# Kernel tuning notes

Hardware: AMD Instinct MI355X
Metric: run time of the kernel (lower is better)

Reference implementation:

```python
import jax, jax.numpy as jnp
import numpy as np

BLOCK_SIZE = 64
N_EMBD = 128
N_HEAD = 4
HEAD_DIM = N_EMBD // N_HEAD  # 32


def setup_inputs() -> dict:
    key = jax.random.key(0)
    kx, kq, kk, kv = jax.random.split(key, 4)
    B, T = 4096, 64
    x = jax.random.normal(kx, (B, T, N_EMBD), dtype=jnp.float32)
    # nn.Linear(n_embd, head_dim, bias=False): stored as [out,in] in torch,
    # here kept as [in, out] = [128, 32] so projection is x @ W.
    s = 1.0 / np.sqrt(N_EMBD)
    Wq = jax.random.uniform(kq, (N_EMBD, HEAD_DIM), jnp.float32, -s, s)
    Wk = jax.random.uniform(kk, (N_EMBD, HEAD_DIM), jnp.float32, -s, s)
    Wv = jax.random.uniform(kv, (N_EMBD, HEAD_DIM), jnp.float32, -s, s)
    return {"x": x, "Wq": Wq, "Wk": Wk, "Wv": Wv}


def reference(x, Wq, Wk, Wv):
    B, T, C = x.shape
    q = x @ Wq  # [B, T, Hd]
    k = x @ Wk
    v = x @ Wv
    scale = 1.0 / jnp.sqrt(jnp.asarray(k.shape[-1], x.dtype))
    wei = jnp.einsum("btd,bsd->bts", q, k) * scale  # [B, T, T]
    causal = jnp.tril(jnp.ones((T, T), dtype=bool))
    wei = jnp.where(causal, wei, -jnp.inf)
    wei = jax.nn.softmax(wei, axis=-1)
    out = jnp.einsum("bts,bsd->btd", wei, v)  # [B, T, Hd]
    return out
```

## Files before the change

### kernel.cpp

```cpp
#include <hip/hip_runtime.h>


#define TT 64
#define CC 128
#define HD 32

typedef __bf16 bf16_t;
typedef __bf16 bf8_t __attribute__((ext_vector_type(8)));
typedef __bf16 bf4_t __attribute__((ext_vector_type(4)));
typedef float  f4_t  __attribute__((ext_vector_type(4)));

__global__ __launch_bounds__(256) void prep_weights(
    const float* __restrict__ Wq, const float* __restrict__ Wk,
    const float* __restrict__ Wv, bf16_t* __restrict__ wf)
{
  int t = blockIdx.x * 256 + threadIdx.x;
  int j    = t & 7;
  int lane = (t >> 3) & 63;
  int kt   = (t >> 9) & 3;
  int n6   = t >> 11;
  int k    = kt * 32 + (lane >> 4) * 8 + j;
  int col  = (n6 & 1) * 16 + (lane & 15);
  const float* W = (n6 >> 1) == 0 ? Wq : ((n6 >> 1) == 1 ? Wk : Wv);
  float v = W[k * HD + col];
  if (n6 < 2) v *= 0.17677669529663687f;
  wf[t] = (bf16_t)v;
}

__global__ __launch_bounds__(64, 2) void head_fused(
    const float* __restrict__ x, const bf8_t* __restrict__ wf,
    float* __restrict__ out)
{
  __shared__ __align__(16) bf16_t qs[TT][40];
  __shared__ __align__(16) bf16_t ks[TT][40];
  __shared__ __align__(16) bf16_t vt[HD][72];
  __shared__ __align__(16) bf16_t ps[16][72];

  const int lane = threadIdx.x;
  const int quad = lane >> 4;
  const int l16  = lane & 15;
  const int b    = blockIdx.x;
  const float* __restrict__ xblk = x + (size_t)b * (TT * CC);
  float* __restrict__ ob = out + (size_t)b * (TT * HD);

  const f4_t zero4 = {0.f, 0.f, 0.f, 0.f};

  bf8_t wfr[24];

  auto load_tile = [&](float4* d, int i) {
    #pragma unroll
    for (int kk = 0; kk < 4; ++kk) {
      const float* s = xblk + (16 * i + l16) * CC + kk * 32 + quad * 8;
      d[2 * kk]     = *(const float4*)s;
      d[2 * kk + 1] = *(const float4*)(s + 4);
    }
  };

  auto proj_tile = [&](const float4* d, int i) {
    f4_t acc[6];
    #pragma unroll
    for (int n = 0; n < 6; ++n) acc[n] = zero4;
    #pragma unroll
    for (int kk = 0; kk < 4; ++kk) {
      float4 f0 = d[2 * kk], f1 = d[2 * kk + 1];
      bf8_t a;
      a[0] = (bf16_t)f0.x; a[1] = (bf16_t)f0.y; a[2] = (bf16_t)f0.z; a[3] = (bf16_t)f0.w;
      a[4] = (bf16_t)f1.x; a[5] = (bf16_t)f1.y; a[6] = (bf16_t)f1.z; a[7] = (bf16_t)f1.w;
      #pragma unroll
      for (int n = 0; n < 6; ++n)
        acc[n] = __builtin_amdgcn_mfma_f32_16x16x32_bf16(a, wfr[n * 4 + kk], acc[n], 0, 0, 0);
    }
    #pragma unroll
    for (int r = 0; r < 4; ++r) {
      int row = 16 * i + quad * 4 + r;
      qs[row][l16]      = (bf16_t)acc[0][r];
      qs[row][16 + l16] = (bf16_t)acc[1][r];
      ks[row][l16]      = (bf16_t)acc[2][r];
      ks[row][16 + l16] = (bf16_t)acc[3][r];
    }
    bf4_t v0 = { (bf16_t)acc[4][0], (bf16_t)acc[4][1], (bf16_t)acc[4][2], (bf16_t)acc[4][3] };
    bf4_t v1 = { (bf16_t)acc[5][0], (bf16_t)acc[5][1], (bf16_t)acc[5][2], (bf16_t)acc[5][3] };
    *(bf4_t*)&vt[l16][16 * i + quad * 4]      = v0;
    *(bf4_t*)&vt[16 + l16][16 * i + quad * 4] = v1;
  };

  float4 ta[8], tb[8];
  load_tile(ta, 0);
  #pragma unroll
  for (int t = 0; t < 24; ++t) wfr[t] = wf[t * 64 + lane];
  load_tile(tb, 1);
  proj_tile(ta, 0);
  load_tile(ta, 2);
  proj_tile(tb, 1);
  load_tile(tb, 3);
  proj_tile(ta, 2);
  proj_tile(tb, 3);

  #pragma unroll
  for (int i = 0; i < 4; ++i) {
    f4_t sc[4];
    bf8_t aq = *(const bf8_t*)&qs[16 * i + l16][quad * 8];
    #pragma unroll
    for (int j = 0; j < 4; ++j) {
      sc[j] = zero4;
      if (j <= i) {
        bf8_t bk = *(const bf8_t*)&ks[16 * j + l16][quad * 8];
        sc[j] = __builtin_amdgcn_mfma_f32_16x16x32_bf16(aq, bk, zero4, 0, 0, 0);
      }
    }
    #pragma unroll
    for (int r = 0; r < 4; ++r) {
      int rl = quad * 4 + r;
      float p[4];
      float psum = 0.f;
      #pragma unroll
      for (int j = 0; j < 4; ++j) {
        if (j <= i) {
          bool valid = (j < i) | (l16 <= rl);
          float e = __expf(sc[j][r]);
          p[j] = valid ? e : 0.f;
          psum += p[j];
        } else p[j] = 0.f;
      }
      #pragma unroll
      for (int off = 1; off < 16; off <<= 1)
        psum += __shfl_xor(psum, off);
      float inv = __builtin_amdgcn_rcpf(psum);
      #pragma unroll
      for (int j = 0; j < 4; ++j) {
        if (j <= i)             ps[rl][j * 16 + l16] = (bf16_t)(p[j] * inv);
        else if (j == (i | 1))  ps[rl][j * 16 + l16] = (bf16_t)0.f;
      }
    }
    f4_t o0 = zero4, o1 = zero4;
    #pragma unroll
    for (int kk = 0; kk <= (i >> 1); ++kk) {
      int k0 = kk * 32 + quad * 8;
      bf8_t ap  = *(const bf8_t*)&ps[l16][k0];
      bf8_t bv0 = *(const bf8_t*)&vt[l16][k0];
      bf8_t bv1 = *(const bf8_t*)&vt[16 + l16][k0];
      o0 = __builtin_amdgcn_mfma_f32_16x16x32_bf16(ap, bv0, o0, 0, 0, 0);
      o1 = __builtin_amdgcn_mfma_f32_16x16x32_bf16(ap, bv1, o1, 0, 0, 0);
    }
    #pragma unroll
    for (int r = 0; r < 4; ++r) {
      int row = 16 * i + quad * 4 + r;
      ob[row * HD + l16]      = o0[r];
      ob[row * HD + 16 + l16] = o1[r];
    }
  }
}

extern "C" void kernel_launch(void* const* d_in, const int* in_sizes, int n_in,
                              void* d_out, int out_size, void* d_ws, size_t ws_size,
                              hipStream_t stream) {
  const float* x  = (const float*)d_in[0];
  const float* Wq = (const float*)d_in[1];
  const float* Wk = (const float*)d_in[2];
  const float* Wv = (const float*)d_in[3];
  float* out = (float*)d_out;
  bf16_t* wf = (bf16_t*)d_ws;
  int B = in_sizes[0] / (TT * CC);

  prep_weights<<<dim3(48), dim3(256), 0, stream>>>(Wq, Wk, Wv, wf);
  head_fused<<<dim3(B), dim3(64), 0, stream>>>(x, (const bf8_t*)wf, out);
}
```

Baseline: 208.9 us.

## Defer softmax normalization via ones-MFMA row sums and interleave projection with attention

Replaces the per-row shuffle reduction and reciprocal scaling of probabilities with an extra MFMA against a vector of ones, so each row sum comes out of the PV matmul and normalization is applied to the output. It also reorders the schedule so the softmax/PV for the first query tiles runs before the last projection tile, overlapping the final x loads with attention work. The cost is an extra MFMA per PV step. Row sums are now taken from the bf16-rounded unnormalized probabilities, which slightly changes numerics.

```diff
diff --git a/kernel.cpp b/kernel.cpp
--- a/kernel.cpp
+++ b/kernel.cpp
@@ -44,8 +44,12 @@
   float* __restrict__ ob = out + (size_t)b * (TT * HD);
 
   const f4_t zero4 = {0.f, 0.f, 0.f, 0.f};
+  bf8_t ones8;
+  #pragma unroll
+  for (int t = 0; t < 8; ++t) ones8[t] = (bf16_t)1.0f;
 
   bf8_t wfr[24];
+  float4 ta[8], tb[8];
 
   auto load_tile = [&](float4* d, int i) {
     #pragma unroll
@@ -84,20 +88,7 @@
     *(bf4_t*)&vt[16 + l16][16 * i + quad * 4] = v1;
   };
 
-  float4 ta[8], tb[8];
-  load_tile(ta, 0);
-  #pragma unroll
-  for (int t = 0; t < 24; ++t) wfr[t] = wf[t * 64 + lane];
-  load_tile(tb, 1);
-  proj_tile(ta, 0);
-  load_tile(ta, 2);
-  proj_tile(tb, 1);
-  load_tile(tb, 3);
-  proj_tile(ta, 2);
-  proj_tile(tb, 3);
-
-  #pragma unroll
-  for (int i = 0; i < 4; ++i) {
+  auto sm_tile = [&](int i) {
     f4_t sc[4];
     bf8_t aq = *(const bf8_t*)&qs[16 * i + l16][quad * 8];
     #pragma unroll
@@ -111,44 +102,49 @@
     #pragma unroll
     for (int r = 0; r < 4; ++r) {
       int rl = quad * 4 + r;
-      float p[4];
-      float psum = 0.f;
       #pragma unroll
       for (int j = 0; j < 4; ++j) {
         if (j <= i) {
           bool valid = (j < i) | (l16 <= rl);
           float e = __expf(sc[j][r]);
-          p[j] = valid ? e : 0.f;
-          psum += p[j];
-        } else p[j] = 0.f;
-      }
-      #pragma unroll
-      for (int off = 1; off < 16; off <<= 1)
-        psum += __shfl_xor(psum, off);
-      float inv = __builtin_amdgcn_rcpf(psum);
-      #pragma unroll
-      for (int j = 0; j < 4; ++j) {
-        if (j <= i)             ps[rl][j * 16 + l16] = (bf16_t)(p[j] * inv);
-        else if (j == (i | 1))  ps[rl][j * 16 + l16] = (bf16_t)0.f;
+          ps[rl][j * 16 + l16] = (bf16_t)(valid ? e : 0.f);
+        } else if (j == (i | 1)) {
+          ps[rl][j * 16 + l16] = (bf16_t)0.f;
+        }
       }
     }
-    f4_t o0 = zero4, o1 = zero4;
+    f4_t o0 = zero4, o1 = zero4, osum = zero4;
     #pragma unroll
     for (int kk = 0; kk <= (i >> 1); ++kk) {
       int k0 = kk * 32 + quad * 8;
       bf8_t ap  = *(const bf8_t*)&ps[l16][k0];
       bf8_t bv0 = *(const bf8_t*)&vt[l16][k0];
       bf8_t bv1 = *(const bf8_t*)&vt[16 + l16][k0];
-      o0 = __builtin_amdgcn_mfma_f32_16x16x32_bf16(ap, bv0, o0, 0, 0, 0);
-      o1 = __builtin_amdgcn_mfma_f32_16x16x32_bf16(ap, bv1, o1, 0, 0, 0);
+      o0   = __builtin_amdgcn_mfma_f32_16x16x32_bf16(ap, bv0, o0, 0, 0, 0);
+      o1   = __builtin_amdgcn_mfma_f32_16x16x32_bf16(ap, bv1, o1, 0, 0, 0);
+      osum = __builtin_amdgcn_mfma_f32_16x16x32_bf16(ap, ones8, osum, 0, 0, 0);
     }
     #pragma unroll
     for (int r = 0; r < 4; ++r) {
       int row = 16 * i + quad * 4 + r;
-      ob[row * HD + l16]      = o0[r];
-      ob[row * HD + 16 + l16] = o1[r];
+      float inv = __builtin_amdgcn_rcpf(osum[r]);
+      ob[row * HD + l16]      = o0[r] * inv;
+      ob[row * HD + 16 + l16] = o1[r] * inv;
     }
-  }
+  };
+
+  load_tile(ta, 0);
+  #pragma unroll
+  for (int t = 0; t < 24; ++t) wfr[t] = wf[t * 64 + lane];
+  load_tile(tb, 1);
+  proj_tile(ta, 0);  load_tile(ta, 2);
+  proj_tile(tb, 1);  load_tile(tb, 3);
+  proj_tile(ta, 2);
+  sm_tile(0);
+  sm_tile(1);
+  proj_tile(tb, 3);
+  sm_tile(2);
+  sm_tile(3);
 }
 
 extern "C" void kernel_launch(void* const* d_in, const int* in_sizes, int n_in,
```

Measured after the change: 206.3 us. No clear change (-1.2%).
